# Performance work log

Hardware: AMD Instinct MI355X
Metric: run time of the kernel (lower is better)

The kernel has to match this reference:

```python
import jax, jax.numpy as jnp
import numpy as np

WINDOW = 12  # fixed half-window from the original module


def setup_inputs() -> dict:
    key = jax.random.key(0)
    ks = jax.random.split(key, 8)
    B, S, G, H = 8, 512, 16, 128
    Da, Dm = 8 * H, 2 * H
    att = jax.random.normal(ks[0], (B, S, Da), jnp.float32)
    mod = jax.random.normal(ks[1], (B, S, Dm), jnp.float32)
    W_att = jax.random.normal(ks[2], (3 * Da,), jnp.float32) * 0.02
    b_att = jax.random.normal(ks[3], (1,), jnp.float32) * 0.02
    W_mod = jax.random.normal(ks[4], (3 * Dm,), jnp.float32) * 0.02
    b_mod = jax.random.normal(ks[5], (1,), jnp.float32) * 0.02
    q_enc = jax.random.normal(ks[6], (B, 30, Dm), jnp.float32)
    gap_indices = jax.random.randint(ks[7], (B, G), 0, S)
    mask = jnp.ones((B, S), jnp.int32)
    q_mask = jnp.ones((B, 30), jnp.int32)
    return dict(att=att, mod=mod, W_att=W_att, b_att=b_att, W_mod=W_mod,
                b_mod=b_mod, q_enc=q_enc, gap_indices=gap_indices,
                mask=mask, q_mask=q_mask)


def _pools(x, maskf, wmf):
    # x: [B,S,D]; maskf: [B,S] float; wmf: [B,G-1,S] float window masks
    # gap 0: full-sequence pooling (max is unmasked, avg divides by mask sum -- faithful)
    max0 = jnp.max(x, axis=1)                                   # [B,D]
    avg0 = jnp.sum(x, axis=1) / jnp.sum(maskf, axis=1, keepdims=True)
    p0 = jnp.concatenate([max0, avg0], axis=-1)[:, None, :]      # [B,1,2D]
    # remaining gaps: masked windowed max/avg (masked entries zeroed, as in torch)
    s = jnp.einsum('bgs,bsd->bgd', wmf, x)                       # windowed sums
    cnt = jnp.sum(wmf, axis=2, keepdims=True)                    # [B,G-1,1]
    avg = s / cnt
    mx = jnp.max(x[:, None, :, :] * wmf[:, :, :, None], axis=2)  # [B,G-1,D]
    return jnp.concatenate([p0, jnp.concatenate([mx, avg], axis=-1)], axis=1)


def reference(att, mod, W_att, b_att, W_mod, b_mod, q_enc, gap_indices, mask, q_mask):
    B, S, _ = mod.shape
    bidx = jnp.arange(B)[:, None]
    att_gaps = att[bidx, gap_indices]   # [B,G,Da]
    mod_gaps = mod[bidx, gap_indices]   # [B,G,Dm]

    maskf = mask.astype(jnp.float32)
    gaps_rest = gap_indices[:, 1:]      # [B,G-1]
    idx = jnp.arange(S)
    wm = ((idx[None, None, :] >= gaps_rest[:, :, None] - WINDOW)
          & (idx[None, None, :] <= gaps_rest[:, :, None] + WINDOW)
          & (mask[:, None, :] > 0))
    wmf = wm.astype(jnp.float32)        # [B,G-1,S]

    pools_att = _pools(att, maskf, wmf)  # [B,G,2*Da]
    pools_mod = _pools(mod, maskf, wmf)  # [B,G,2*Dm]

    att_cat = jnp.concatenate([att_gaps, pools_att], axis=-1)  # [B,G,3*Da]
    mod_cat = jnp.concatenate([mod_gaps, pools_mod], axis=-1)  # [B,G,3*Dm]

    logits = (jnp.einsum('bgd,d->bg', att_cat, W_att) + b_att
              + jnp.einsum('bgd,d->bg', mod_cat, W_mod) + b_mod)
    return logits  # [B,G]
```

## Files before the change

### kernel.cpp

```cpp
#include <hip/hip_runtime.h>
#include <math.h>

#define B 8
#define S 512
#define G 16
#define DA 1024
#define DM 256
#define WIN 12
#define NCH 32
#define RPC (S / NCH)
#define DTOT (DA + DM)
#define NW 8
#define RPW (RPC / NW)
#define NWIN (B * (G - 1))
#define NBLK1 (NWIN + NCH * B)

__inline__ __device__ float4 fmax4(float4 a, float4 b) {
    return make_float4(fmaxf(a.x, b.x), fmaxf(a.y, b.y),
                       fmaxf(a.z, b.z), fmaxf(a.w, b.w));
}
__inline__ __device__ float4 add4(float4 a, float4 b) {
    return make_float4(a.x + b.x, a.y + b.y, a.z + b.z, a.w + b.w);
}
__inline__ __device__ float dot4(float4 a, float4 b) {
    return a.x * b.x + a.y * b.y + a.z * b.z + a.w * b.w;
}

__inline__ __device__ float4 blockReduceSum4_8(float4 v, float4* sh) {
    int lane = threadIdx.x & 63, w = threadIdx.x >> 6;
#pragma unroll
    for (int o = 32; o > 0; o >>= 1) {
        v.x += __shfl_xor(v.x, o, 64);
        v.y += __shfl_xor(v.y, o, 64);
        v.z += __shfl_xor(v.z, o, 64);
        v.w += __shfl_xor(v.w, o, 64);
    }
    __syncthreads();
    if (lane == 0) sh[w] = v;
    __syncthreads();
    float4 r = sh[0];
#pragma unroll
    for (int ww = 1; ww < 8; ++ww) {
        r.x += sh[ww].x; r.y += sh[ww].y; r.z += sh[ww].z; r.w += sh[ww].w;
    }
    return r;
}

__global__ __launch_bounds__(512) void k_main(
    const float* __restrict__ att, const float* __restrict__ mod,
    const float* __restrict__ Wa, const float* __restrict__ Wm,
    const float* __restrict__ ba, const float* __restrict__ bm,
    const int* __restrict__ gidx, const int* __restrict__ mask,
    float* __restrict__ pmax, float* __restrict__ psum,
    float* __restrict__ out)
{
    __shared__ float part[NW][DTOT];
    __shared__ float4 s4[NW];
    const int bid = blockIdx.x;
    const int t = threadIdx.x, lane = t & 63, w = t >> 6;

    const float4* att4 = (const float4*)att;
    const float4* mod4 = (const float4*)mod;

    if (bid >= NWIN) {
        const int sid = bid - NWIN;
        const int b = sid >> 5, ch = sid & (NCH - 1);

        float4 amax[4], asum[4];
#pragma unroll
        for (int k = 0; k < 4; ++k) {
            amax[k] = make_float4(-INFINITY, -INFINITY, -INFINITY, -INFINITY);
            asum[k] = make_float4(0.f, 0.f, 0.f, 0.f);
        }
        float4 mmax = make_float4(-INFINITY, -INFINITY, -INFINITY, -INFINITY);
        float4 msum = make_float4(0.f, 0.f, 0.f, 0.f);

        const int row0 = b * S + ch * RPC + w * RPW;
#pragma unroll
        for (int r = 0; r < RPW; ++r) {
            const float4* arow = att4 + (size_t)(row0 + r) * (DA / 4);
#pragma unroll
            for (int k = 0; k < 4; ++k) {
                float4 v = arow[lane + 64 * k];
                amax[k] = fmax4(amax[k], v);
                asum[k] = add4(asum[k], v);
            }
            float4 vm = mod4[(size_t)(row0 + r) * (DM / 4) + lane];
            mmax = fmax4(mmax, vm);
            msum = add4(msum, vm);
        }

        const size_t base = ((size_t)b * NCH + ch) * DTOT;
        float4* pr = (float4*)&part[w][0];

#pragma unroll
        for (int k = 0; k < 4; ++k) pr[lane + 64 * k] = amax[k];
        ((float4*)&part[w][DA])[lane] = mmax;
        __syncthreads();
        for (int d = t; d < DTOT; d += 512) {
            float mx = part[0][d];
#pragma unroll
            for (int ww = 1; ww < NW; ++ww) mx = fmaxf(mx, part[ww][d]);
            pmax[base + d] = mx;
        }
        __syncthreads();

#pragma unroll
        for (int k = 0; k < 4; ++k) pr[lane + 64 * k] = asum[k];
        ((float4*)&part[w][DA])[lane] = msum;
        __syncthreads();
        for (int d = t; d < DTOT; d += 512) {
            float sm = part[0][d];
#pragma unroll
            for (int ww = 1; ww < NW; ++ww) sm += part[ww][d];
            psum[base + d] = sm;
        }
    } else {
        const int b = bid / (G - 1), g = 1 + bid % (G - 1);
        const int gi = gidx[b * G + g];

        float cd = 0.f;
        if (t < 256)
            cd = dot4(att4[(size_t)(b * S + gi) * (DA / 4) + t],
                      ((const float4*)Wa)[t]);
        else if (t < 256 + DM / 4)
            cd = dot4(mod4[(size_t)(b * S + gi) * (DM / 4) + (t - 256)],
                      ((const float4*)Wm)[t - 256]);

        int lo = gi - WIN; if (lo < 0) lo = 0;
        int hi = gi + WIN; if (hi > S - 1) hi = S - 1;

        float4 amax2[4], asum2[4];
#pragma unroll
        for (int k = 0; k < 4; ++k) {
            amax2[k] = make_float4(0.f, 0.f, 0.f, 0.f);
            asum2[k] = make_float4(0.f, 0.f, 0.f, 0.f);
        }
        float4 mmax2 = make_float4(0.f, 0.f, 0.f, 0.f);
        float4 msum2 = make_float4(0.f, 0.f, 0.f, 0.f);
        float cn = 0.f;

        for (int s = lo + w; s <= hi; s += NW) {
            if (mask[b * S + s] > 0) {
                const int row = b * S + s;
                const float4* arow = att4 + (size_t)row * (DA / 4);
#pragma unroll
                for (int k = 0; k < 4; ++k) {
                    float4 v = arow[lane + 64 * k];
                    amax2[k] = fmax4(amax2[k], v);
                    asum2[k] = add4(asum2[k], v);
                }
                float4 vm = mod4[(size_t)row * (DM / 4) + lane];
                mmax2 = fmax4(mmax2, vm);
                msum2 = add4(msum2, vm);
                if (lane == 0) cn += 1.f;
            }
        }

        float4* pr = (float4*)&part[w][0];

#pragma unroll
        for (int k = 0; k < 4; ++k) pr[lane + 64 * k] = amax2[k];
        ((float4*)&part[w][DA])[lane] = mmax2;
        __syncthreads();
        float wdot1 = 0.f;
        for (int d = t; d < DTOT; d += 512) {
            float mx = part[0][d];
#pragma unroll
            for (int ww = 1; ww < 8; ++ww) mx = fmaxf(mx, part[ww][d]);
            float wgt = (d < DA) ? Wa[DA + d] : Wm[DM + (d - DA)];
            wdot1 += wgt * mx;
        }
        __syncthreads();

#pragma unroll
        for (int k = 0; k < 4; ++k) pr[lane + 64 * k] = asum2[k];
        ((float4*)&part[w][DA])[lane] = msum2;
        __syncthreads();
        float wdot2 = 0.f;
        for (int d = t; d < DTOT; d += 512) {
            float sm = part[0][d];
#pragma unroll
            for (int ww = 1; ww < 8; ++ww) sm += part[ww][d];
            float wgt = (d < DA) ? Wa[2 * DA + d] : Wm[2 * DM + (d - DA)];
            wdot2 += wgt * sm;
        }

        float4 r = blockReduceSum4_8(make_float4(wdot1, wdot2, cd, cn), s4);
        if (t == 0)
            out[b * G + g] = r.z + r.x + r.y / r.w + ba[0] + bm[0];
    }
}

__global__ __launch_bounds__(512) void k_g0(
    const float* __restrict__ att, const float* __restrict__ mod,
    const float* __restrict__ Wa, const float* __restrict__ Wm,
    const float* __restrict__ ba, const float* __restrict__ bm,
    const int* __restrict__ gidx, const int* __restrict__ mask,
    const float* __restrict__ pmax, const float* __restrict__ psum,
    float* __restrict__ out)
{
    __shared__ float pM[NW][64], pS[NW][64];
    __shared__ float4 s4[NW];
    const int c = blockIdx.x, b = blockIdx.y;
    const int t = threadIdx.x, lane = t & 63, w = t >> 6;

    float cmv = (float)mask[b * S + t];
    float cm = blockReduceSum4_8(make_float4(cmv, 0.f, 0.f, 0.f), s4).x;

    if (c < 20) {
        const int d = c * 64 + lane;
        float mx = -INFINITY, sm = 0.f;
#pragma unroll
        for (int k = 0; k < NCH / NW; ++k) {
            const int ch = w + NW * k;
            const size_t o = ((size_t)b * NCH + ch) * DTOT + d;
            mx = fmaxf(mx, pmax[o]);
            sm += psum[o];
        }
        pM[w][lane] = mx;
        pS[w][lane] = sm;
        __syncthreads();

        float val = 0.f;
        if (t < 64) {
            float m2 = pM[0][t], s2 = pS[0][t];
#pragma unroll
            for (int ww = 1; ww < NW; ++ww) {
                m2 = fmaxf(m2, pM[ww][t]);
                s2 += pS[ww][t];
            }
            const int d2 = c * 64 + t;
            float w1 = (d2 < DA) ? Wa[DA + d2] : Wm[DM + (d2 - DA)];
            float w2 = (d2 < DA) ? Wa[2 * DA + d2] : Wm[2 * DM + (d2 - DA)];
            val = w1 * m2 + w2 * (s2 / cm);
        }
        if (w == 0) {
#pragma unroll
            for (int o = 32; o > 0; o >>= 1) val += __shfl_xor(val, o, 64);
            if (lane == 0) atomicAdd(&out[b * G], val);
        }
    } else {
        const int gi = gidx[b * G];
        const float4* att4 = (const float4*)att;
        const float4* mod4 = (const float4*)mod;
        float cd = 0.f;
        if (t < 256)
            cd = dot4(att4[(size_t)(b * S + gi) * (DA / 4) + t],
                      ((const float4*)Wa)[t]);
        else if (t < 256 + DM / 4)
            cd = dot4(mod4[(size_t)(b * S + gi) * (DM / 4) + (t - 256)],
                      ((const float4*)Wm)[t - 256]);
        float4 r = blockReduceSum4_8(make_float4(cd, 0.f, 0.f, 0.f), s4);
        if (t == 0) atomicAdd(&out[b * G], r.x + ba[0] + bm[0]);
    }
}

extern "C" void kernel_launch(void* const* d_in, const int* in_sizes, int n_in,
                              void* d_out, int out_size, void* d_ws, size_t ws_size,
                              hipStream_t stream) {
    const float* att  = (const float*)d_in[0];
    const float* mod  = (const float*)d_in[1];
    const float* Wa   = (const float*)d_in[2];
    const float* ba   = (const float*)d_in[3];
    const float* Wm   = (const float*)d_in[4];
    const float* bm   = (const float*)d_in[5];
    const int* gidx   = (const int*)d_in[7];
    const int* mask   = (const int*)d_in[8];
    float* out = (float*)d_out;

    float* ws   = (float*)d_ws;
    float* pmax = ws;
    float* psum = pmax + (size_t)B * NCH * DTOT;

    hipMemsetAsync(out, 0, (size_t)out_size * sizeof(float), stream);
    k_main<<<NBLK1, 512, 0, stream>>>(att, mod, Wa, Wm, ba, bm, gidx, mask,
                                      pmax, psum, out);
    k_g0<<<dim3(21, B), 512, 0, stream>>>(att, mod, Wa, Wm, ba, bm, gidx, mask,
                                          pmax, psum, out);
}
```

Baseline: 21.41 us.

## Fuse gap-0 finalization into main kernel via last-block atomic counter

Removes the second kernel launch and the output memset. Each batch's last finishing sweep block now does the gap-0 reduction over the per-chunk partials, detected with an atomic counter, and writes the logit directly instead of accumulating it with atomics. Sweep blocks are also moved to the front of the grid so they are scheduled first. The trade-off is that one block per batch does the whole 32-chunk reduction serially, and correctness depends on a counter in uninitialized workspace, using a modulo trick so it keeps working across calls.

```diff
diff --git a/kernel.cpp b/kernel.cpp
--- a/kernel.cpp
+++ b/kernel.cpp
@@ -12,8 +12,9 @@
 #define DTOT (DA + DM)
 #define NW 8
 #define RPW (RPC / NW)
+#define NSWEEP (NCH * B)
 #define NWIN (B * (G - 1))
-#define NBLK1 (NWIN + NCH * B)
+#define NBLK (NSWEEP + NWIN)
 
 __inline__ __device__ float4 fmax4(float4 a, float4 b) {
     return make_float4(fmaxf(a.x, b.x), fmaxf(a.y, b.y),
@@ -52,19 +53,19 @@
     const float* __restrict__ ba, const float* __restrict__ bm,
     const int* __restrict__ gidx, const int* __restrict__ mask,
     float* __restrict__ pmax, float* __restrict__ psum,
-    float* __restrict__ out)
+    unsigned int* __restrict__ cnt, float* __restrict__ out)
 {
     __shared__ float part[NW][DTOT];
     __shared__ float4 s4[NW];
+    __shared__ int isLast;
     const int bid = blockIdx.x;
     const int t = threadIdx.x, lane = t & 63, w = t >> 6;
 
     const float4* att4 = (const float4*)att;
     const float4* mod4 = (const float4*)mod;
 
-    if (bid >= NWIN) {
-        const int sid = bid - NWIN;
-        const int b = sid >> 5, ch = sid & (NCH - 1);
+    if (bid < NSWEEP) {
+        const int b = bid >> 5, ch = bid & (NCH - 1);
 
         float4 amax[4], asum[4];
 #pragma unroll
@@ -115,8 +116,50 @@
             for (int ww = 1; ww < NW; ++ww) sm += part[ww][d];
             psum[base + d] = sm;
         }
+
+        __threadfence();
+        __syncthreads();
+        if (t == 0) {
+            unsigned int old = __hip_atomic_fetch_add(
+                &cnt[b], 1u, __ATOMIC_ACQ_REL, __HIP_MEMORY_SCOPE_AGENT);
+            isLast = ((old & (NCH - 1u)) == NCH - 1u) ? 1 : 0;
+        }
+        __syncthreads();
+        if (!isLast) return;
+
+        __threadfence();
+
+        float cmv = (float)mask[b * S + t];
+
+        const int gi = gidx[b * G];
+        float cd = 0.f;
+        if (t < 256)
+            cd = dot4(att4[(size_t)(b * S + gi) * (DA / 4) + t],
+                      ((const float4*)Wa)[t]);
+        else if (t < 256 + DM / 4)
+            cd = dot4(mod4[(size_t)(b * S + gi) * (DM / 4) + (t - 256)],
+                      ((const float4*)Wm)[t - 256]);
+
+        float gd1 = 0.f, gd2 = 0.f;
+        for (int d = t; d < DTOT; d += 512) {
+            float mx = -INFINITY, sm = 0.f;
+#pragma unroll 8
+            for (int c2 = 0; c2 < NCH; ++c2) {
+                const size_t o = ((size_t)b * NCH + c2) * DTOT + d;
+                mx = fmaxf(mx, pmax[o]);
+                sm += psum[o];
+            }
+            float wg1 = (d < DA) ? Wa[DA + d] : Wm[DM + (d - DA)];
+            float wg2 = (d < DA) ? Wa[2 * DA + d] : Wm[2 * DM + (d - DA)];
+            gd1 += wg1 * mx;
+            gd2 += wg2 * sm;
+        }
+        float4 r = blockReduceSum4_8(make_float4(gd1, gd2, cd, cmv), s4);
+        if (t == 0)
+            out[b * G + 0] = r.z + r.x + r.y / r.w + ba[0] + bm[0];
     } else {
-        const int b = bid / (G - 1), g = 1 + bid % (G - 1);
+        const int idx = bid - NSWEEP;
+        const int b = idx / (G - 1), g = 1 + idx % (G - 1);
         const int gi = gidx[b * G + g];
 
         float cd = 0.f;
@@ -189,70 +232,6 @@
         float4 r = blockReduceSum4_8(make_float4(wdot1, wdot2, cd, cn), s4);
         if (t == 0)
             out[b * G + g] = r.z + r.x + r.y / r.w + ba[0] + bm[0];
-    }
-}
-
-__global__ __launch_bounds__(512) void k_g0(
-    const float* __restrict__ att, const float* __restrict__ mod,
-    const float* __restrict__ Wa, const float* __restrict__ Wm,
-    const float* __restrict__ ba, const float* __restrict__ bm,
-    const int* __restrict__ gidx, const int* __restrict__ mask,
-    const float* __restrict__ pmax, const float* __restrict__ psum,
-    float* __restrict__ out)
-{
-    __shared__ float pM[NW][64], pS[NW][64];
-    __shared__ float4 s4[NW];
-    const int c = blockIdx.x, b = blockIdx.y;
-    const int t = threadIdx.x, lane = t & 63, w = t >> 6;
-
-    float cmv = (float)mask[b * S + t];
-    float cm = blockReduceSum4_8(make_float4(cmv, 0.f, 0.f, 0.f), s4).x;
-
-    if (c < 20) {
-        const int d = c * 64 + lane;
-        float mx = -INFINITY, sm = 0.f;
-#pragma unroll
-        for (int k = 0; k < NCH / NW; ++k) {
-            const int ch = w + NW * k;
-            const size_t o = ((size_t)b * NCH + ch) * DTOT + d;
-            mx = fmaxf(mx, pmax[o]);
-            sm += psum[o];
-        }
-        pM[w][lane] = mx;
-        pS[w][lane] = sm;
-        __syncthreads();
-
-        float val = 0.f;
-        if (t < 64) {
-            float m2 = pM[0][t], s2 = pS[0][t];
-#pragma unroll
-            for (int ww = 1; ww < NW; ++ww) {
-                m2 = fmaxf(m2, pM[ww][t]);
-                s2 += pS[ww][t];
-            }
-            const int d2 = c * 64 + t;
-            float w1 = (d2 < DA) ? Wa[DA + d2] : Wm[DM + (d2 - DA)];
-            float w2 = (d2 < DA) ? Wa[2 * DA + d2] : Wm[2 * DM + (d2 - DA)];
-            val = w1 * m2 + w2 * (s2 / cm);
-        }
-        if (w == 0) {
-#pragma unroll
-            for (int o = 32; o > 0; o >>= 1) val += __shfl_xor(val, o, 64);
-            if (lane == 0) atomicAdd(&out[b * G], val);
-        }
-    } else {
-        const int gi = gidx[b * G];
-        const float4* att4 = (const float4*)att;
-        const float4* mod4 = (const float4*)mod;
-        float cd = 0.f;
-        if (t < 256)
-            cd = dot4(att4[(size_t)(b * S + gi) * (DA / 4) + t],
-                      ((const float4*)Wa)[t]);
-        else if (t < 256 + DM / 4)
-            cd = dot4(mod4[(size_t)(b * S + gi) * (DM / 4) + (t - 256)],
-                      ((const float4*)Wm)[t - 256]);
-        float4 r = blockReduceSum4_8(make_float4(cd, 0.f, 0.f, 0.f), s4);
-        if (t == 0) atomicAdd(&out[b * G], r.x + ba[0] + bm[0]);
     }
 }
 
@@ -272,10 +251,8 @@
     float* ws   = (float*)d_ws;
     float* pmax = ws;
     float* psum = pmax + (size_t)B * NCH * DTOT;
-
-    hipMemsetAsync(out, 0, (size_t)out_size * sizeof(float), stream);
-    k_main<<<NBLK1, 512, 0, stream>>>(att, mod, Wa, Wm, ba, bm, gidx, mask,
-                                      pmax, psum, out);
-    k_g0<<<dim3(21, B), 512, 0, stream>>>(att, mod, Wa, Wm, ba, bm, gidx, mask,
-                                          pmax, psum, out);
-}
+    unsigned int* cnt = (unsigned int*)(psum + (size_t)B * NCH * DTOT);
+
+    k_main<<<NBLK, 512, 0, stream>>>(att, mod, Wa, Wm, ba, bm, gidx, mask,
+                                     pmax, psum, cnt, out);
+}
```

New measurement: 66.61 us. +211.1%, slower.
